# Performance work log

Measured on AMD Instinct MI355X. Metric: run time of the kernel, lower is better.

The kernel has to match this reference:

```python
import jax, jax.numpy as jnp
import numpy as np

B, T, V, H = 16, 128, 32000, 768
P = H // 2
NBOW = 64
PAD = 0
EPS = 0.05     # label smoothing
TAU = 0.07
W_CE, W_AL, W_BOW, W_DIV, W_VAR = 1.0, 0.5, 0.2, 0.1, 0.05
BOW_IDS = jnp.arange(NBOW, dtype=jnp.int32) * 500  # registered buffer bow_indices_tensor


def _ln(x, g, b):
    m = jnp.mean(x, axis=-1, keepdims=True)
    v = jnp.mean((x - m) ** 2, axis=-1, keepdims=True)
    return (x - m) / jnp.sqrt(v + 1e-5) * g + b


def _l2norm(x):
    return x / jnp.maximum(jnp.linalg.norm(x, axis=-1, keepdims=True), 1e-12)


def _proj(x, g, bn, W1, b1, W2, b2):
    h = _ln(x, g, bn)
    h = jax.nn.gelu(h @ W1 + b1, approximate=False)  # torch nn.GELU default = exact
    return h @ W2 + b2


def setup_inputs() -> dict:
    key = jax.random.key(0)
    ks = jax.random.split(key, 12)
    s = 0.02
    return {
        "logits": jax.random.normal(ks[0], (B, T, V), dtype=jnp.float32),
        "labels": jax.random.randint(ks[1], (B, T), 0, V, dtype=jnp.int32),
        "attention_mask": jnp.ones((B, T), dtype=jnp.int32),
        "encoder_features": jax.random.normal(ks[2], (B, H), dtype=jnp.float32),
        "decoder_hidden": jax.random.normal(ks[3], (B, T, H), dtype=jnp.float32),
        "ln_g_e": jnp.ones((H,), jnp.float32), "ln_b_e": jnp.zeros((H,), jnp.float32),
        "W1_e": jax.random.normal(ks[4], (H, P), jnp.float32) * s, "b1_e": jnp.zeros((P,), jnp.float32),
        "W2_e": jax.random.normal(ks[5], (P, P), jnp.float32) * s, "b2_e": jnp.zeros((P,), jnp.float32),
        "ln_g_t": jnp.ones((H,), jnp.float32), "ln_b_t": jnp.zeros((H,), jnp.float32),
        "W1_t": jax.random.normal(ks[6], (H, P), jnp.float32) * s, "b1_t": jnp.zeros((P,), jnp.float32),
        "W2_t": jax.random.normal(ks[7], (P, P), jnp.float32) * s, "b2_t": jnp.zeros((P,), jnp.float32),
        "W_bow": jax.random.normal(ks[8], (H, NBOW), jnp.float32) * s, "b_bow": jnp.zeros((NBOW,), jnp.float32),
    }


def _forward(logits, labels, attention_mask, encoder_features, decoder_hidden,
             ln_g_e, ln_b_e, W1_e, b1_e, W2_e, b2_e,
             ln_g_t, ln_b_t, W1_t, b1_t, W2_t, b2_t,
             W_bow, b_bow):
    # --- label-smoothed CE over valid (non-pad, non -100) tokens ---
    valid = (labels != PAD) & (labels != -100)                      # (B,T)
    lab = jnp.clip(labels, 0, V - 1)
    lp = jax.nn.log_softmax(logits, axis=-1)                        # (B,T,V)
    lp_lab = jnp.take_along_axis(lp, lab[..., None], axis=-1)[..., 0]
    tok_loss = -((1.0 - EPS) * lp_lab + (EPS / V) * lp.sum(-1))     # smooth target = (1-eps) at label + eps/V everywhere
    vf = valid.astype(jnp.float32)
    ce = (tok_loss * vf).sum() / jnp.maximum(vf.sum(), 1.0)

    # --- contrastive alignment (InfoNCE both ways) ---
    m = attention_mask[..., None].astype(jnp.float32)               # (B,T,1)
    pooled = (decoder_hidden * m).sum(1) / jnp.maximum(m.sum(1), 1.0)
    z_e = _l2norm(_proj(encoder_features, ln_g_e, ln_b_e, W1_e, b1_e, W2_e, b2_e))
    z_t = _l2norm(_proj(pooled, ln_g_t, ln_b_t, W1_t, b1_t, W2_t, b2_t))
    sim = (z_e @ z_t.T) / TAU                                       # (B,B)
    li = -jnp.diag(jax.nn.log_softmax(sim, axis=-1)).mean()
    lj = -jnp.diag(jax.nn.log_softmax(sim.T, axis=-1)).mean()
    align = 0.5 * (li + lj)

    # --- BoW BCE: target[b,i] = any valid token of row b equals bow id i ---
    match = (lab[:, :, None] == BOW_IDS[None, None, :]) & valid[:, :, None]
    bow_t = match.any(axis=1).astype(jnp.float32)                   # (B,NBOW)
    bl = encoder_features @ W_bow + b_bow
    bce = jnp.mean(jnp.maximum(bl, 0.0) - bl * bow_t + jnp.log1p(jnp.exp(-jnp.abs(bl))))

    # --- diversity: mean |off-diagonal cosine sim| of encoder features ---
    nf = _l2norm(encoder_features)
    sm = nf @ nf.T
    off = 1.0 - jnp.eye(B, dtype=jnp.float32)
    div = (jnp.abs(sm) * off).sum() / (B * B - B)

    # --- variance: mean exp(-var_dim) (torch.var uses ddof=1) ---
    fvar = jnp.var(encoder_features, axis=0, ddof=1)
    var_l = jnp.mean(jnp.exp(-fvar))

    return W_CE * ce + W_AL * align + W_BOW * bce + W_DIV * div + W_VAR * var_l


def reference(logits, labels, attention_mask, encoder_features, decoder_hidden,
              ln_g_e, ln_b_e, W1_e, b1_e, W2_e, b2_e,
              ln_g_t, ln_b_t, W1_t, b1_t, W2_t, b2_t,
              W_bow, b_bow):
    return _forward(logits, labels, attention_mask, encoder_features, decoder_hidden,
                    ln_g_e, ln_b_e, W1_e, b1_e, W2_e, b2_e,
                    ln_g_t, ln_b_t, W1_t, b1_t, W2_t, b2_t,
                    W_bow, b_bow)
```

## Files before the change

kernel.cpp:

```cpp
#include <hip/hip_runtime.h>
#include <math.h>

#define BB 16
#define TT 128
#define VV 32000
#define HH 768
#define PP 384
#define NBOWD 64
#define EPS_LS 0.05f
#define TAUC 0.07f
#define SMALLB 50

__device__ __forceinline__ float blockReduceSum256(float v, float* sh) {
  int tid = threadIdx.x;
  sh[tid] = v;
  __syncthreads();
  for (int s = 128; s > 0; s >>= 1) {
    if (tid < s) sh[tid] += sh[tid + s];
    __syncthreads();
  }
  float r = sh[0];
  __syncthreads();
  return r;
}

__global__ __launch_bounds__(256) void fused_main(
    const float* __restrict__ logits, const int* __restrict__ labels, const int* __restrict__ amask,
    const float* __restrict__ enc, const float* __restrict__ dh,
    const float* __restrict__ g_e, const float* __restrict__ be_, const float* __restrict__ W1e,
    const float* __restrict__ b1e, const float* __restrict__ W2e, const float* __restrict__ b2e,
    const float* __restrict__ g_t, const float* __restrict__ bt_, const float* __restrict__ W1t,
    const float* __restrict__ b1t, const float* __restrict__ W2t, const float* __restrict__ b2t,
    const float* __restrict__ W_bow, const float* __restrict__ b_bow,
    float* __restrict__ tok, float* __restrict__ vfs,
    float* __restrict__ ze, float* __restrict__ zt,
    float* __restrict__ bce_p, float* __restrict__ div_p, float* __restrict__ var_p) {
  __shared__ float smem[1792];
  int tid = threadIdx.x;
  int blk = blockIdx.x;

  if (blk >= SMALLB) {
    int row = blk - SMALLB;
    const float* x = logits + (size_t)row * VV;
    const float4* x4 = (const float4*)x;
    float m = -INFINITY, s = 0.f, sx = 0.f;
    for (int k = tid; k < VV / 4; k += 256) {
      float4 v = x4[k];
      float lm = fmaxf(fmaxf(v.x, v.y), fmaxf(v.z, v.w));
      float ls = __expf(v.x - lm) + __expf(v.y - lm) + __expf(v.z - lm) + __expf(v.w - lm);
      sx += (v.x + v.y) + (v.z + v.w);
      float nm = fmaxf(m, lm);
      s = s * __expf(m - nm) + ls * __expf(lm - nm);
      m = nm;
    }
    float* sm_ = smem;
    float* ss_ = smem + 256;
    float* sxa = smem + 512;
    sm_[tid] = m; ss_[tid] = s; sxa[tid] = sx;
    __syncthreads();
    for (int o = 128; o > 0; o >>= 1) {
      if (tid < o) {
        float m2 = sm_[tid + o], s2 = ss_[tid + o];
        float nm = fmaxf(sm_[tid], m2);
        ss_[tid] = ss_[tid] * __expf(sm_[tid] - nm) + s2 * __expf(m2 - nm);
        sm_[tid] = nm;
        sxa[tid] += sxa[tid + o];
      }
      __syncthreads();
    }
    if (tid == 0) {
      float M = sm_[0], L = logf(ss_[0]), SX = sxa[0];
      int lab = labels[row];
      bool valid = (lab != 0) && (lab != -100);
      int lc = lab < 0 ? 0 : (lab > VV - 1 ? VV - 1 : lab);
      float xl = x[lc];
      float lp_lab = xl - M - L;
      float lp_sum = SX - (float)VV * (M + L);
      float tl = -((1.f - EPS_LS) * lp_lab + (EPS_LS / (float)VV) * lp_sum);
      tok[row] = valid ? tl : 0.f;
      vfs[row] = valid ? 1.f : 0.f;
    }
    return;
  }

  if (blk < 32) {
    float* xs = smem;
    float* hs = smem + 768;
    float* red = smem + 1152;
    float* mf = smem + 1408;
    float* mden = smem + 1536;
    bool is_t = blk >= BB;
    int b = blk & (BB - 1);
    const float *g, *bb_, *W1, *b1, *W2, *b2;
    float* zout;
    if (is_t) { g = g_t; bb_ = bt_; W1 = W1t; b1 = b1t; W2 = W2t; b2 = b2t; zout = zt; }
    else      { g = g_e; bb_ = be_; W1 = W1e; b1 = b1e; W2 = W2e; b2 = b2e; zout = ze; }

    if (is_t) {
      if (tid < TT) mf[tid] = (float)amask[b * TT + tid];
      __syncthreads();
      if (tid == 0) {
        float sum = 0.f;
        for (int t = 0; t < TT; t++) sum += mf[t];
        mden[0] = fmaxf(sum, 1.f);
      }
      __syncthreads();
      const float* dbase = dh + (size_t)b * TT * HH;
      for (int h = tid; h < HH; h += 256) {
        float acc = 0.f;
        for (int t = 0; t < TT; t++) acc += dbase[t * HH + h] * mf[t];
        xs[h] = acc / mden[0];
      }
    } else {
      for (int k = tid; k < HH; k += 256) xs[k] = enc[b * HH + k];
    }
    __syncthreads();

    float s1 = 0.f, s2 = 0.f;
    for (int k = tid; k < HH; k += 256) { float v = xs[k]; s1 += v; s2 += v * v; }
    s1 = blockReduceSum256(s1, red);
    s2 = blockReduceSum256(s2, red);
    float mean = s1 / (float)HH;
    float var = s2 / (float)HH - mean * mean;
    float rstd = rsqrtf(var + 1e-5f);
    for (int k = tid; k < HH; k += 256) xs[k] = (xs[k] - mean) * rstd * g[k] + bb_[k];
    __syncthreads();

    for (int j = tid; j < PP; j += 256) {
      float acc = b1[j];
      for (int k = 0; k < HH; k++) acc += xs[k] * W1[k * PP + j];
      hs[j] = 0.5f * acc * (1.f + erff(acc * 0.70710678118654752440f));
    }
    __syncthreads();
    for (int j = tid; j < PP; j += 256) {
      float acc = b2[j];
      for (int k = 0; k < PP; k++) acc += hs[k] * W2[k * PP + j];
      red[0];
      xs[j] = acc;
    }
    __syncthreads();
    float sq = 0.f;
    for (int j = tid; j < PP; j += 256) { float v = xs[j]; sq += v * v; }
    sq = blockReduceSum256(sq, red);
    float inv = 1.f / fmaxf(sqrtf(sq), 1e-12f);
    for (int j = tid; j < PP; j += 256) zout[b * PP + j] = xs[j] * inv;
    return;
  }

  if (blk < 48) {
    int b = blk - 32;
    int iw = tid & 63, p = tid >> 6;
    int* labs = (int*)(smem + 512);
    if (tid < TT) labs[tid] = labels[b * TT + tid];
    const float* er = enc + b * HH;
    float acc = 0.f;
    for (int k = p * 192; k < (p + 1) * 192; k++) acc += er[k] * W_bow[k * NBOWD + iw];
    smem[p * 64 + iw] = acc;
    __syncthreads();
    if (tid < 64) {
      float bl = b_bow[iw] + smem[iw] + smem[64 + iw] + smem[128 + iw] + smem[192 + iw];
      int target = 0, idv = iw * 500;
      for (int t = 0; t < TT; t++) {
        int lab = labs[t];
        if (lab != 0 && lab != -100) {
          int lc = lab < 0 ? 0 : (lab > VV - 1 ? VV - 1 : lab);
          if (lc == idv) target = 1;
        }
      }
      smem[256 + iw] = fmaxf(bl, 0.f) - bl * (float)target + log1pf(__expf(-fabsf(bl)));
    }
    __syncthreads();
    if (tid == 0) {
      float s = 0.f;
      for (int i = 0; i < 64; i++) s += smem[256 + i];
      bce_p[b] = s;
    }
    return;
  }

  if (blk == 48) {
    int i = tid >> 4, j = tid & 15;
    const float* a = enc + i * HH;
    const float* c = enc + j * HH;
    float d = 0.f;
    for (int k = 0; k < HH; k++) d += a[k] * c[k];
    smem[tid] = d;
    __syncthreads();
    float contrib = 0.f;
    if (i != j) {
      float ni = fmaxf(sqrtf(smem[i * 17]), 1e-12f);
      float nj = fmaxf(sqrtf(smem[j * 17]), 1e-12f);
      contrib = fabsf(smem[tid]) / (ni * nj);
    }
    float r = blockReduceSum256(contrib, smem + 256);
    if (tid == 0) div_p[0] = r / (float)(BB * BB - BB);
    return;
  }

  {
    float vsum = 0.f;
    for (int d = tid; d < HH; d += 256) {
      float a1 = 0.f, a2 = 0.f;
      for (int b = 0; b < BB; b++) { float v = enc[b * HH + d]; a1 += v; a2 += v * v; }
      float mean = a1 / (float)BB;
      float vr = (a2 - (float)BB * mean * mean) / (float)(BB - 1);
      vsum += __expf(-vr);
    }
    float r = blockReduceSum256(vsum, smem);
    if (tid == 0) var_p[0] = r / (float)HH;
  }
}

__global__ __launch_bounds__(256) void finalize2(
    const float* __restrict__ tok, const float* __restrict__ vfs,
    const float* __restrict__ ze, const float* __restrict__ zt,
    const float* __restrict__ bce_p, const float* __restrict__ div_p, const float* __restrict__ var_p,
    float* __restrict__ out) {
  __shared__ float sh[256];
  __shared__ float smat[256];
  __shared__ float misc[40];
  int tid = threadIdx.x;

  float tsum = 0.f, csum = 0.f;
  for (int i = tid; i < BB * TT; i += 256) { tsum += tok[i]; csum += vfs[i]; }
  float ce_sum = blockReduceSum256(tsum, sh);
  float ce_cnt = blockReduceSum256(csum, sh);

  {
    int i = tid >> 4, j = tid & 15;
    const float* a = ze + i * PP;
    const float* c = zt + j * PP;
    float d = 0.f;
    for (int k = 0; k < PP; k++) d += a[k] * c[k];
    smat[tid] = d * (1.f / TAUC);
  }
  __syncthreads();
  if (tid < 32) {
    bool isrow = tid < 16;
    int r = tid & 15;
    float mx = -1e30f;
    for (int j = 0; j < 16; j++) { float v = isrow ? smat[r * 16 + j] : smat[j * 16 + r]; mx = fmaxf(mx, v); }
    float se = 0.f;
    for (int j = 0; j < 16; j++) { float v = isrow ? smat[r * 16 + j] : smat[j * 16 + r]; se += __expf(v - mx); }
    misc[tid] = smat[r * 17] - mx - logf(se);
  }
  __syncthreads();
  if (tid == 0) {
    float li = 0.f, lj = 0.f;
    for (int r = 0; r < 16; r++) { li += misc[r]; lj += misc[16 + r]; }
    float align = 0.5f * (-(li / 16.f) - (lj / 16.f));
    float bce = 0.f;
    for (int b = 0; b < BB; b++) bce += bce_p[b];
    bce /= (float)(BB * NBOWD);
    float ce = ce_sum / fmaxf(ce_cnt, 1.f);
    out[0] = 1.0f * ce + 0.5f * align + 0.2f * bce + 0.1f * div_p[0] + 0.05f * var_p[0];
  }
}

extern "C" void kernel_launch(void* const* d_in, const int* in_sizes, int n_in,
                              void* d_out, int out_size, void* d_ws, size_t ws_size,
                              hipStream_t stream) {
  const float* logits = (const float*)d_in[0];
  const int* labels   = (const int*)d_in[1];
  const int* amask    = (const int*)d_in[2];
  const float* enc    = (const float*)d_in[3];
  const float* dh     = (const float*)d_in[4];
  const float* g_e    = (const float*)d_in[5];
  const float* be_    = (const float*)d_in[6];
  const float* W1e    = (const float*)d_in[7];
  const float* b1e    = (const float*)d_in[8];
  const float* W2e    = (const float*)d_in[9];
  const float* b2e    = (const float*)d_in[10];
  const float* g_t    = (const float*)d_in[11];
  const float* bt_    = (const float*)d_in[12];
  const float* W1t    = (const float*)d_in[13];
  const float* b1t    = (const float*)d_in[14];
  const float* W2t    = (const float*)d_in[15];
  const float* b2t    = (const float*)d_in[16];
  const float* W_bow  = (const float*)d_in[17];
  const float* b_bow  = (const float*)d_in[18];

  float* f   = (float*)d_ws;
  float* tok = f;
  float* vfs = f + 2048;
  float* ze  = f + 4096;
  float* zt  = f + 10240;
  float* bce_p = f + 16384;
  float* div_p = f + 16400;
  float* var_p = f + 16401;

  fused_main<<<SMALLB + BB * TT, 256, 0, stream>>>(
      logits, labels, amask, enc, dh,
      g_e, be_, W1e, b1e, W2e, b2e,
      g_t, bt_, W1t, b1t, W2t, b2t,
      W_bow, b_bow, tok, vfs, ze, zt, bce_p, div_p, var_p);
  finalize2<<<1, 256, 0, stream>>>(tok, vfs, ze, zt, bce_p, div_p, var_p, (float*)d_out);
}
```

Before: 505.7 us.

## Unroll CE row loop and split BOW/diversity work across more blocks

Rewrites the per-row logsumexp loop as a fully unrolled set of four independent online-softmax accumulators with several float4 loads in flight, which exposes more memory-level parallelism. The BOW matvec and encoder Gram matrix are split into K-chunks across more blocks, and their final reductions, label-target flags, BCE and diversity are moved into the finalize kernel. The projection matvecs and the decoder masked mean get multiple accumulators and unrolling. The cost is more workspace and more work in the single-block finalize kernel.

```diff
diff --git a/kernel.cpp b/kernel.cpp
--- a/kernel.cpp
+++ b/kernel.cpp
@@ -9,7 +9,7 @@
 #define NBOWD 64
 #define EPS_LS 0.05f
 #define TAUC 0.07f
-#define SMALLB 50
+#define SMALLB 101
 
 __device__ __forceinline__ float blockReduceSum256(float v, float* sh) {
   int tid = threadIdx.x;
@@ -22,6 +22,14 @@
   float r = sh[0];
   __syncthreads();
   return r;
+}
+
+__device__ __forceinline__ void ce_upd(float& m, float& s, float& sx, float4 v) {
+  sx += (v.x + v.y) + (v.z + v.w);
+  float lm = fmaxf(fmaxf(v.x, v.y), fmaxf(v.z, v.w));
+  float nm = fmaxf(m, lm);
+  s = s * __expf(m - nm) + __expf(v.x - nm) + __expf(v.y - nm) + __expf(v.z - nm) + __expf(v.w - nm);
+  m = nm;
 }
 
 __global__ __launch_bounds__(256) void fused_main(
@@ -34,7 +42,7 @@
     const float* __restrict__ W_bow, const float* __restrict__ b_bow,
     float* __restrict__ tok, float* __restrict__ vfs,
     float* __restrict__ ze, float* __restrict__ zt,
-    float* __restrict__ bce_p, float* __restrict__ div_p, float* __restrict__ var_p) {
+    float* __restrict__ bowp, float* __restrict__ divp, float* __restrict__ var_p) {
   __shared__ float smem[1792];
   int tid = threadIdx.x;
   int blk = blockIdx.x;
@@ -43,16 +51,25 @@
     int row = blk - SMALLB;
     const float* x = logits + (size_t)row * VV;
     const float4* x4 = (const float4*)x;
-    float m = -INFINITY, s = 0.f, sx = 0.f;
-    for (int k = tid; k < VV / 4; k += 256) {
-      float4 v = x4[k];
-      float lm = fmaxf(fmaxf(v.x, v.y), fmaxf(v.z, v.w));
-      float ls = __expf(v.x - lm) + __expf(v.y - lm) + __expf(v.z - lm) + __expf(v.w - lm);
-      sx += (v.x + v.y) + (v.z + v.w);
-      float nm = fmaxf(m, lm);
-      s = s * __expf(m - nm) + ls * __expf(lm - nm);
-      m = nm;
-    }
+    float m0 = -INFINITY, m1 = -INFINITY, m2 = -INFINITY, m3 = -INFINITY;
+    float s0 = 0.f, s1 = 0.f, s2 = 0.f, s3 = 0.f, sx = 0.f;
+#pragma unroll
+    for (int g = 0; g < 8; ++g) {
+      int base = (g << 10) + tid;
+      float4 v0 = x4[base];
+      float4 v1 = x4[base + 256];
+      float4 v2 = x4[base + 512];
+      ce_upd(m0, s0, sx, v0);
+      ce_upd(m1, s1, sx, v1);
+      ce_upd(m2, s2, sx, v2);
+      if (g < 7 || tid < 64) {
+        float4 v3 = x4[base + 768];
+        ce_upd(m3, s3, sx, v3);
+      }
+    }
+    float m = fmaxf(fmaxf(m0, m1), fmaxf(m2, m3));
+    float s = s0 * __expf(m0 - m) + s1 * __expf(m1 - m) + s2 * __expf(m2 - m) + s3 * __expf(m3 - m);
+
     float* sm_ = smem;
     float* ss_ = smem + 256;
     float* sxa = smem + 512;
@@ -60,9 +77,9 @@
     __syncthreads();
     for (int o = 128; o > 0; o >>= 1) {
       if (tid < o) {
-        float m2 = sm_[tid + o], s2 = ss_[tid + o];
-        float nm = fmaxf(sm_[tid], m2);
-        ss_[tid] = ss_[tid] * __expf(sm_[tid] - nm) + s2 * __expf(m2 - nm);
+        float m2_ = sm_[tid + o], s2_ = ss_[tid + o];
+        float nm = fmaxf(sm_[tid], m2_);
+        ss_[tid] = ss_[tid] * __expf(sm_[tid] - nm) + s2_ * __expf(m2_ - nm);
         sm_[tid] = nm;
         sxa[tid] += sxa[tid + o];
       }
@@ -107,9 +124,16 @@
       __syncthreads();
       const float* dbase = dh + (size_t)b * TT * HH;
       for (int h = tid; h < HH; h += 256) {
-        float acc = 0.f;
-        for (int t = 0; t < TT; t++) acc += dbase[t * HH + h] * mf[t];
-        xs[h] = acc / mden[0];
+        const float* db = dbase + h;
+        float a0 = 0.f, a1 = 0.f, a2 = 0.f, a3 = 0.f;
+#pragma unroll 8
+        for (int t = 0; t < TT; t += 4) {
+          a0 += db[(t + 0) * HH] * mf[t + 0];
+          a1 += db[(t + 1) * HH] * mf[t + 1];
+          a2 += db[(t + 2) * HH] * mf[t + 2];
+          a3 += db[(t + 3) * HH] * mf[t + 3];
+        }
+        xs[h] = ((a0 + a1) + (a2 + a3)) / mden[0];
       }
     } else {
       for (int k = tid; k < HH; k += 256) xs[k] = enc[b * HH + k];
@@ -127,16 +151,24 @@
     __syncthreads();
 
     for (int j = tid; j < PP; j += 256) {
-      float acc = b1[j];
-      for (int k = 0; k < HH; k++) acc += xs[k] * W1[k * PP + j];
+      float a0 = 0.f, a1 = 0.f;
+#pragma unroll 8
+      for (int k = 0; k < HH; k += 2) {
+        a0 += xs[k] * W1[k * PP + j];
+        a1 += xs[k + 1] * W1[(k + 1) * PP + j];
+      }
+      float acc = b1[j] + a0 + a1;
       hs[j] = 0.5f * acc * (1.f + erff(acc * 0.70710678118654752440f));
     }
     __syncthreads();
     for (int j = tid; j < PP; j += 256) {
-      float acc = b2[j];
-      for (int k = 0; k < PP; k++) acc += hs[k] * W2[k * PP + j];
-      red[0];
-      xs[j] = acc;
+      float a0 = 0.f, a1 = 0.f;
+#pragma unroll 8
+      for (int k = 0; k < PP; k += 2) {
+        a0 += hs[k] * W2[k * PP + j];
+        a1 += hs[k + 1] * W2[(k + 1) * PP + j];
+      }
+      xs[j] = b2[j] + a0 + a1;
     }
     __syncthreads();
     float sq = 0.f;
@@ -147,53 +179,33 @@
     return;
   }
 
-  if (blk < 48) {
-    int b = blk - 32;
-    int iw = tid & 63, p = tid >> 6;
-    int* labs = (int*)(smem + 512);
-    if (tid < TT) labs[tid] = labels[b * TT + tid];
+  if (blk < 96) {
+    int bb = blk - 32;
+    int b = bb >> 2, kq = bb & 3;
+    int iw = tid & 63, ks = tid >> 6;
     const float* er = enc + b * HH;
+    int k0 = kq * 192 + ks * 48;
     float acc = 0.f;
-    for (int k = p * 192; k < (p + 1) * 192; k++) acc += er[k] * W_bow[k * NBOWD + iw];
-    smem[p * 64 + iw] = acc;
-    __syncthreads();
-    if (tid < 64) {
-      float bl = b_bow[iw] + smem[iw] + smem[64 + iw] + smem[128 + iw] + smem[192 + iw];
-      int target = 0, idv = iw * 500;
-      for (int t = 0; t < TT; t++) {
-        int lab = labs[t];
-        if (lab != 0 && lab != -100) {
-          int lc = lab < 0 ? 0 : (lab > VV - 1 ? VV - 1 : lab);
-          if (lc == idv) target = 1;
-        }
-      }
-      smem[256 + iw] = fmaxf(bl, 0.f) - bl * (float)target + log1pf(__expf(-fabsf(bl)));
-    }
-    __syncthreads();
-    if (tid == 0) {
-      float s = 0.f;
-      for (int i = 0; i < 64; i++) s += smem[256 + i];
-      bce_p[b] = s;
-    }
+#pragma unroll 8
+    for (int k = 0; k < 48; ++k) acc += er[k0 + k] * W_bow[(k0 + k) * NBOWD + iw];
+    smem[ks * 64 + iw] = acc;
+    __syncthreads();
+    if (tid < 64) bowp[bb * 64 + tid] = smem[tid] + smem[64 + tid] + smem[128 + tid] + smem[192 + tid];
     return;
   }
 
-  if (blk == 48) {
+  if (blk < 100) {
+    int kq = blk - 96;
     int i = tid >> 4, j = tid & 15;
-    const float* a = enc + i * HH;
-    const float* c = enc + j * HH;
-    float d = 0.f;
-    for (int k = 0; k < HH; k++) d += a[k] * c[k];
-    smem[tid] = d;
-    __syncthreads();
-    float contrib = 0.f;
-    if (i != j) {
-      float ni = fmaxf(sqrtf(smem[i * 17]), 1e-12f);
-      float nj = fmaxf(sqrtf(smem[j * 17]), 1e-12f);
-      contrib = fabsf(smem[tid]) / (ni * nj);
-    }
-    float r = blockReduceSum256(contrib, smem + 256);
-    if (tid == 0) div_p[0] = r / (float)(BB * BB - BB);
+    const float* a = enc + i * HH + kq * 192;
+    const float* c = enc + j * HH + kq * 192;
+    float a0 = 0.f, a1 = 0.f;
+#pragma unroll 8
+    for (int k = 0; k < 192; k += 2) {
+      a0 += a[k] * c[k];
+      a1 += a[k + 1] * c[k + 1];
+    }
+    divp[kq * 256 + tid] = a0 + a1;
     return;
   }
 
@@ -201,6 +213,7 @@
     float vsum = 0.f;
     for (int d = tid; d < HH; d += 256) {
       float a1 = 0.f, a2 = 0.f;
+#pragma unroll
       for (int b = 0; b < BB; b++) { float v = enc[b * HH + d]; a1 += v; a2 += v * v; }
       float mean = a1 / (float)BB;
       float vr = (a2 - (float)BB * mean * mean) / (float)(BB - 1);
@@ -214,12 +227,27 @@
 __global__ __launch_bounds__(256) void finalize2(
     const float* __restrict__ tok, const float* __restrict__ vfs,
     const float* __restrict__ ze, const float* __restrict__ zt,
-    const float* __restrict__ bce_p, const float* __restrict__ div_p, const float* __restrict__ var_p,
+    const float* __restrict__ bowp, const float* __restrict__ divp, const float* __restrict__ var_p,
+    const int* __restrict__ labels, const float* __restrict__ b_bow,
     float* __restrict__ out) {
   __shared__ float sh[256];
   __shared__ float smat[256];
   __shared__ float misc[40];
+  __shared__ int flags[BB * NBOWD];
   int tid = threadIdx.x;
+
+  for (int i = tid; i < BB * NBOWD; i += 256) flags[i] = 0;
+  __syncthreads();
+  for (int i = tid; i < BB * TT; i += 256) {
+    int lab = labels[i];
+    if (lab != 0 && lab != -100) {
+      int lc = lab < 0 ? 0 : (lab > VV - 1 ? VV - 1 : lab);
+      if (lc % 500 == 0) {
+        int iw = lc / 500;
+        if (iw < NBOWD) flags[(i >> 7) * NBOWD + iw] = 1;
+      }
+    }
+  }
 
   float tsum = 0.f, csum = 0.f;
   for (int i = tid; i < BB * TT; i += 256) { tsum += tok[i]; csum += vfs[i]; }
@@ -230,9 +258,10 @@
     int i = tid >> 4, j = tid & 15;
     const float* a = ze + i * PP;
     const float* c = zt + j * PP;
-    float d = 0.f;
-    for (int k = 0; k < PP; k++) d += a[k] * c[k];
-    smat[tid] = d * (1.f / TAUC);
+    float a0 = 0.f, a1 = 0.f;
+#pragma unroll 8
+    for (int k = 0; k < PP; k += 2) { a0 += a[k] * c[k]; a1 += a[k + 1] * c[k + 1]; }
+    smat[tid] = (a0 + a1) * (1.f / TAUC);
   }
   __syncthreads();
   if (tid < 32) {
@@ -245,15 +274,42 @@
     misc[tid] = smat[r * 17] - mx - logf(se);
   }
   __syncthreads();
+  float align;
   if (tid == 0) {
     float li = 0.f, lj = 0.f;
     for (int r = 0; r < 16; r++) { li += misc[r]; lj += misc[16 + r]; }
-    float align = 0.5f * (-(li / 16.f) - (lj / 16.f));
-    float bce = 0.f;
-    for (int b = 0; b < BB; b++) bce += bce_p[b];
-    bce /= (float)(BB * NBOWD);
+    misc[33] = 0.5f * (-(li / 16.f) - (lj / 16.f));
+  }
+  __syncthreads();
+  align = misc[33];
+  __syncthreads();
+
+  float bsum = 0.f;
+  for (int e = tid; e < BB * NBOWD; e += 256) {
+    int b = e >> 6, iw = e & 63;
+    float bl = b_bow[iw] + bowp[(b * 4 + 0) * 64 + iw] + bowp[(b * 4 + 1) * 64 + iw]
+             + bowp[(b * 4 + 2) * 64 + iw] + bowp[(b * 4 + 3) * 64 + iw];
+    float tgt = (float)flags[e];
+    bsum += fmaxf(bl, 0.f) - bl * tgt + log1pf(__expf(-fabsf(bl)));
+  }
+  float bce = blockReduceSum256(bsum, sh) / (float)(BB * NBOWD);
+
+  smat[tid] = divp[tid] + divp[256 + tid] + divp[512 + tid] + divp[768 + tid];
+  __syncthreads();
+  float contrib = 0.f;
+  {
+    int i = tid >> 4, j = tid & 15;
+    if (i != j) {
+      float ni = fmaxf(sqrtf(smat[i * 17]), 1e-12f);
+      float nj = fmaxf(sqrtf(smat[j * 17]), 1e-12f);
+      contrib = fabsf(smat[tid]) / (ni * nj);
+    }
+  }
+  float divs = blockReduceSum256(contrib, sh) / (float)(BB * BB - BB);
+
+  if (tid == 0) {
     float ce = ce_sum / fmaxf(ce_cnt, 1.f);
-    out[0] = 1.0f * ce + 0.5f * align + 0.2f * bce + 0.1f * div_p[0] + 0.05f * var_p[0];
+    out[0] = 1.0f * ce + 0.5f * align + 0.2f * bce + 0.1f * divs + 0.05f * var_p[0];
   }
 }
 
@@ -280,19 +336,19 @@
   const float* W_bow  = (const float*)d_in[17];
   const float* b_bow  = (const float*)d_in[18];
 
-  float* f   = (float*)d_ws;
-  float* tok = f;
-  float* vfs = f + 2048;
-  float* ze  = f + 4096;
-  float* zt  = f + 10240;
-  float* bce_p = f + 16384;
-  float* div_p = f + 16400;
-  float* var_p = f + 16401;
+  float* f     = (float*)d_ws;
+  float* tok   = f;
+  float* vfs   = f + 2048;
+  float* ze    = f + 4096;
+  float* zt    = f + 10240;
+  float* bowp  = f + 16384;
+  float* divp  = f + 20480;
+  float* var_p = f + 21504;
 
   fused_main<<<SMALLB + BB * TT, 256, 0, stream>>>(
       logits, labels, amask, enc, dh,
       g_e, be_, W1e, b1e, W2e, b2e,
       g_t, bt_, W1t, b1t, W2t, b2t,
-      W_bow, b_bow, tok, vfs, ze, zt, bce_p, div_p, var_p);
-  finalize2<<<1, 256, 0, stream>>>(tok, vfs, ze, zt, bce_p, div_p, var_p, (float*)d_out);
-}
+      W_bow, b_bow, tok, vfs, ze, zt, bowp, divp, var_p);
+  finalize2<<<1, 256, 0, stream>>>(tok, vfs, ze, zt, bowp, divp, var_p, labels, b_bow, (float*)d_out);
+}
```

After: 474.5 us. 1.07x faster.
